# Performance work log

Hardware: AMD Instinct MI355X
Metric: run time of the kernel (lower is better)

The kernel has to match this reference:

```python
import jax, jax.numpy as jnp
import numpy as np

INPUT_DIM = 1024
GRID_SIZE = 5
SPLINE_ORDER = 3
GRID_MIN, GRID_MAX = -1.5, 1.5
NUM_BASIS = GRID_SIZE + SPLINE_ORDER  # 8
LN_EPS = 1e-5


def _spline_grid():
    # grid = arange(-spline_order, grid_size+spline_order+1)*h + grid_min, per input dim
    h = (GRID_MAX - GRID_MIN) / GRID_SIZE
    g = jnp.arange(-SPLINE_ORDER, GRID_SIZE + SPLINE_ORDER + 1, dtype=jnp.float32) * h + GRID_MIN  # [12]
    return jnp.broadcast_to(g, (INPUT_DIM, g.shape[0]))  # [D, 12]


def _rbf_grid():
    return jnp.linspace(GRID_MIN, GRID_MAX, NUM_BASIS, dtype=jnp.float32)  # [8]


def _b_splines(x):
    # x: [B, D] -> bases [B, D, grid_size+spline_order]
    grid = _spline_grid()  # [D, G]
    xe = x[..., None]  # [B, D, 1]
    bases = ((xe >= grid[:, :-1]) & (xe < grid[:, 1:])).astype(x.dtype)  # [B, D, G-1]
    for k in range(1, SPLINE_ORDER + 1):
        left = (xe - grid[:, :-(k + 1)]) / (grid[:, k:-1] - grid[:, :-(k + 1)])
        right = (grid[:, k + 1:] - xe) / (grid[:, k + 1:] - grid[:, 1:-k])
        bases = left * bases[:, :, :-1] + right * bases[:, :, 1:]
    return bases  # [B, D, NUM_BASIS]


def setup_inputs() -> dict:
    key = jax.random.key(0)
    k1, k2, k3 = jax.random.split(key, 3)
    B, D, O = 8192, INPUT_DIM, 1024
    x = jax.random.normal(k1, (B, D), dtype=jnp.float32)
    ln_weight = jnp.ones((D,), dtype=jnp.float32)
    ln_bias = jnp.zeros((D,), dtype=jnp.float32)
    # kaiming_uniform(a=sqrt(5)) ~ U(-1/sqrt(fan_in), 1/sqrt(fan_in))
    base_weight = jax.random.uniform(k2, (O, D), jnp.float32, -1.0, 1.0) / np.sqrt(D)
    spline_weight = jax.random.uniform(k3, (O, D * NUM_BASIS), jnp.float32, -1.0, 1.0) / np.sqrt(D * NUM_BASIS)
    return {"x": x, "ln_weight": ln_weight, "ln_bias": ln_bias,
            "base_weight": base_weight, "spline_weight": spline_weight}


def reference(x, ln_weight, ln_bias, base_weight, spline_weight):
    B = x.shape[0]
    # LayerNorm
    mu = jnp.mean(x, axis=-1, keepdims=True)
    var = jnp.mean((x - mu) ** 2, axis=-1, keepdims=True)
    xn = (x - mu) * jax.lax.rsqrt(var + LN_EPS) * ln_weight + ln_bias  # [B, D]
    # base branch: SiLU + linear
    base_out = jax.nn.silu(xn) @ base_weight.T  # [B, O]
    # spline branch
    spl = _b_splines(xn).reshape(B, -1)  # [B, D*8]
    spline_out = spl @ spline_weight.T
    # rbf branch (same weight)
    denom = (GRID_MAX - GRID_MIN) / (NUM_BASIS - 1)
    rbf = jnp.exp(-(((xn[..., None] - _rbf_grid()) / denom) ** 2)).reshape(B, -1)  # [B, D*8]
    rbf_out = rbf @ spline_weight.T
    return base_out + rbf_out + spline_out
```

## Files before the change

### kernel.cpp

```cpp
#include <hip/hip_runtime.h>

#define B_ROWS 8192
#define D_IN   1024
#define NOUT   1024
#define KB     1024
#define KS     8192
#define GM     256
#define GN     128
#define GK     64
#define GKS    128

#define TBL_N  2048
#define TBL_X0 (-5.5f)
#define TBL_W  11.0f

typedef __attribute__((ext_vector_type(4))) float f32x4;
typedef __attribute__((ext_vector_type(4))) int   i32x4;
typedef __attribute__((ext_vector_type(8))) short bf16x8;

#define SCALE_F 63.5f
#define SCALE_W 11494.728f

__device__ __forceinline__ unsigned short f2bf(float f) {
  union { float f; unsigned u; } v; v.f = f;
  unsigned r = v.u + 0x7fffu + ((v.u >> 16) & 1u);
  return (unsigned short)(r >> 16);
}

__device__ __forceinline__ unsigned pk4(float a, float b, float c, float d, float s) {
  int qa = (int)rintf(fminf(fmaxf(a * s, -127.f), 127.f));
  int qb = (int)rintf(fminf(fmaxf(b * s, -127.f), 127.f));
  int qc = (int)rintf(fminf(fmaxf(c * s, -127.f), 127.f));
  int qd = (int)rintf(fminf(fmaxf(d * s, -127.f), 127.f));
  return (unsigned)(qa & 255) | ((unsigned)(qb & 255) << 8) |
         ((unsigned)(qc & 255) << 16) | ((unsigned)(qd & 255) << 24);
}

__device__ __forceinline__ void load_lds16(const void* g, void* l) {
  __builtin_amdgcn_global_load_lds(
      (const __attribute__((address_space(1))) unsigned int*)g,
      (__attribute__((address_space(3))) unsigned int*)l, 16, 0, 0);
}

__device__ __forceinline__ void barrier_raw() {
  asm volatile("" ::: "memory");
  __builtin_amdgcn_s_barrier();
  asm volatile("" ::: "memory");
}

__global__ __launch_bounds__(256) void tbl_kernel(unsigned char* __restrict__ T) {
  const int k = blockIdx.x * 256 + threadIdx.x;
  const float xn = TBL_X0 + (TBL_W / TBL_N) * k;
  float b[11];
#pragma unroll
  for (int j = 0; j < 11; ++j) {
    const float gj = 0.6f * j - 3.3f;
    b[j] = (xn >= gj && xn < gj + 0.6f) ? 1.f : 0.f;
  }
#pragma unroll
  for (int kk = 1; kk <= 3; ++kk) {
    const float inv = 1.f / (0.6f * kk);
#pragma unroll
    for (int j = 0; j <= 10 - kk; ++j) {
      const float gj = 0.6f * j - 3.3f;
      b[j] = (xn - gj) * inv * b[j] + (gj + 0.6f * (kk + 1) - xn) * inv * b[j + 1];
    }
  }
  float f[8];
#pragma unroll
  for (int j = 0; j < 8; ++j) {
    const float c = -1.5f + (3.f / 7.f) * j;
    const float tt = (xn - c) * (7.f / 3.f);
    f[j] = b[j] + __expf(-tt * tt);
  }
  *reinterpret_cast<uint2*>(T + (size_t)k * 8) =
      make_uint2(pk4(f[0], f[1], f[2], f[3], SCALE_F),
                 pk4(f[4], f[5], f[6], f[7], SCALE_F));
}

__global__ __launch_bounds__(256) void wconv_b(
    const float* __restrict__ bw, unsigned short* __restrict__ Wb) {
  const size_t idx = ((size_t)blockIdx.x * 256 + threadIdx.x) * 4;
  float4 f = *reinterpret_cast<const float4*>(bw + idx);
  union { unsigned short us[4]; uint2 u2; } o;
  o.us[0] = f2bf(f.x); o.us[1] = f2bf(f.y); o.us[2] = f2bf(f.z); o.us[3] = f2bf(f.w);
  *reinterpret_cast<uint2*>(Wb + idx) = o.u2;
}

__global__ __launch_bounds__(256) void wconv_s(
    const float* __restrict__ sw, unsigned char* __restrict__ Ws) {
  const size_t base = ((size_t)blockIdx.x * 256 + threadIdx.x) * 8;
  float4 v0 = *reinterpret_cast<const float4*>(sw + base);
  float4 v1 = *reinterpret_cast<const float4*>(sw + base + 4);
  *reinterpret_cast<uint2*>(Ws + base) =
      make_uint2(pk4(v0.x, v0.y, v0.z, v0.w, SCALE_W),
                 pk4(v1.x, v1.y, v1.z, v1.w, SCALE_W));
}

__global__ __launch_bounds__(256) void feat_kernel(
    const float* __restrict__ x, const float* __restrict__ lnw,
    const float* __restrict__ lnb, const unsigned char* __restrict__ T,
    unsigned short* __restrict__ Fb, unsigned char* __restrict__ Fs, int row0) {
  const int row = row0 + blockIdx.x;
  const float* xr = x + (size_t)row * D_IN;
  const int t = threadIdx.x;
  float v[4];
  float s = 0.f, s2 = 0.f;
#pragma unroll
  for (int i = 0; i < 4; ++i) {
    v[i] = xr[t + 256 * i];
    s += v[i];
    s2 += v[i] * v[i];
  }
#pragma unroll
  for (int off = 32; off > 0; off >>= 1) {
    s += __shfl_xor(s, off);
    s2 += __shfl_xor(s2, off);
  }
  __shared__ float red[8];
  const int wid = t >> 6;
  if ((t & 63) == 0) { red[wid] = s; red[4 + wid] = s2; }
  __syncthreads();
  s  = red[0] + red[1] + red[2] + red[3];
  s2 = red[4] + red[5] + red[6] + red[7];
  const float mu = s * (1.f / D_IN);
  const float var = s2 * (1.f / D_IN) - mu * mu;
  const float rstd = rsqrtf(var + 1e-5f);
  unsigned short* fbr = Fb + (size_t)blockIdx.x * KB;
  unsigned char*  fsr = Fs + (size_t)blockIdx.x * KS;
#pragma unroll
  for (int i = 0; i < 4; ++i) {
    const int d = t + 256 * i;
    const float xn = (v[i] - mu) * rstd * lnw[d] + lnb[d];
    const float e = __expf(-xn);
    fbr[d] = f2bf(xn * __builtin_amdgcn_rcpf(1.f + e));
    int ti = (int)rintf((xn - TBL_X0) * (TBL_N / TBL_W));
    ti = min(max(ti, 0), TBL_N - 1);
    *reinterpret_cast<uint2*>(fsr + d * 8) =
        *reinterpret_cast<const uint2*>(T + (size_t)ti * 8);
  }
}

__global__ __launch_bounds__(512, 2) void gemm_base(
    const unsigned short* __restrict__ A, const unsigned short* __restrict__ Bw,
    float* __restrict__ C, int row0) {
  __shared__ unsigned short As[3][GM * GK];
  __shared__ unsigned short Bs[3][GN * GK];
  const int t = threadIdx.x;
  const int w = t >> 6, l = t & 63;
  const int wr = w >> 1, wc = w & 1;
  const int id = blockIdx.x;
  const int nbm = gridDim.x >> 3;
  int bm, bn;
  if ((nbm & 7) == 0) {
    const int c = id & 7, j = id >> 3, q = nbm >> 3;
    bm = c + 8 * (j % q);
    bn = j / q;
  } else { bm = id % nbm; bn = id / nbm; }
  const size_t Abase = (size_t)bm * GM * KB;
  const size_t Bbase = (size_t)bn * GN * KB;
  const int arow = l >> 3;
  const int achk = (l & 7) ^ arow;
  f32x4 acc[4][4] = {};
  auto stageA = [&](int buf, int k0) {
#pragma unroll
    for (int i = 0; i < 4; ++i) {
      const int seg = w * 4 + i;
      load_lds16(A + Abase + (size_t)(seg * 8 + arow) * KB + k0 + achk * 8,
                 (char*)&As[buf][0] + seg * 1024);
    }
  };
  auto stageB = [&](int buf, int k0) {
#pragma unroll
    for (int i = 0; i < 2; ++i) {
      const int seg = w * 2 + i;
      load_lds16(Bw + Bbase + (size_t)(seg * 8 + arow) * KB + k0 + achk * 8,
                 (char*)&Bs[buf][0] + seg * 1024);
    }
  };
  const int hi = l >> 4;
  const int rA = wr * 64 + (l & 15);
  const int rB = wc * 64 + (l & 15);
  const int rs = l & 7;
  auto dsread = [&](int buf, int kk, bf16x8* a, bf16x8* b) {
    const int cb = ((kk * 4 + hi) ^ rs) * 16;
#pragma unroll
    for (int m = 0; m < 4; ++m)
      a[m] = *reinterpret_cast<const bf16x8*>(
          (const char*)&As[buf][0] + (rA + m * 16) * 128 + cb);
#pragma unroll
    for (int n = 0; n < 4; ++n)
      b[n] = *reinterpret_cast<const bf16x8*>(
          (const char*)&Bs[buf][0] + (rB + n * 16) * 128 + cb);
  };
  auto domfma = [&](bf16x8* a, bf16x8* b) {
    __builtin_amdgcn_s_setprio(1);
#pragma unroll
    for (int m = 0; m < 4; ++m)
#pragma unroll
      for (int n = 0; n < 4; ++n)
        acc[m][n] = __builtin_amdgcn_mfma_f32_16x16x32_bf16(a[m], b[n], acc[m][n], 0, 0, 0);
    __builtin_amdgcn_s_setprio(0);
  };
  const int NT = KB / GK;
  stageA(0, 0); stageB(0, 0);
  stageA(1, GK); stageB(1, GK);
  asm volatile("s_waitcnt vmcnt(6)" ::: "memory");
  barrier_raw();
  int cur = 0;
  for (int tt = 0; tt < NT; ++tt) {
    int pre = cur + 2; if (pre >= 3) pre -= 3;
    const bool have2 = (tt + 2 < NT);
    bf16x8 a0[4], b0[4], a1[4], b1[4];
    dsread(cur, 0, a0, b0);
    dsread(cur, 1, a1, b1);
    if (have2) { stageA(pre, (tt + 2) * GK); stageB(pre, (tt + 2) * GK); }
    __builtin_amdgcn_sched_barrier(0);
    domfma(a0, b0);
    __builtin_amdgcn_sched_barrier(0);
    domfma(a1, b1);
    if (tt + 1 < NT) {
      if (have2) asm volatile("s_waitcnt vmcnt(6)" ::: "memory");
      else       asm volatile("s_waitcnt vmcnt(0)" ::: "memory");
      barrier_raw();
    }
    cur = cur + 1; if (cur >= 3) cur = 0;
  }
  const int crow0 = row0 + bm * GM + wr * 64 + hi * 4;
  const int ccol0 = bn * GN + wc * 64 + (l & 15);
#pragma unroll
  for (int m = 0; m < 4; ++m)
#pragma unroll
    for (int n = 0; n < 4; ++n) {
      float* cp = C + (size_t)(crow0 + m * 16) * NOUT + ccol0 + n * 16;
#pragma unroll
      for (int r = 0; r < 4; ++r)
        cp[(size_t)r * NOUT] = acc[m][n][r];
    }
}

__global__ __launch_bounds__(512, 2) void gemm_spline(
    const unsigned char* __restrict__ Fs, const unsigned char* __restrict__ Ws,
    float* __restrict__ C, int row0) {
  __shared__ __align__(16) unsigned char As[3][GM * GKS];
  __shared__ __align__(16) unsigned char Bs[3][GN * GKS];
  const int t = threadIdx.x;
  const int w = t >> 6, l = t & 63;
  const int wr = w >> 1, wc = w & 1;
  const int id = blockIdx.x;
  const int nbm = gridDim.x >> 3;
  int bm, bn;
  if ((nbm & 7) == 0) {
    const int c = id & 7, j = id >> 3, q = nbm >> 3;
    bm = c + 8 * (j % q);
    bn = j / q;
  } else { bm = id % nbm; bn = id / nbm; }
  const size_t Ab = (size_t)bm * GM * KS;
  const size_t Bb = (size_t)bn * GN * KS;
  i32x4 acc[4][4] = {};
  auto stageA = [&](int buf, int k0) {
#pragma unroll
    for (int i = 0; i < 4; ++i) {
      const int ch = i * 512 + t;
      const int r = ch >> 3, c = ch & 7;
      load_lds16(Fs + Ab + (size_t)r * KS + k0 + ((c ^ (r & 7)) * 16),
                 (char*)&As[buf][0] + ch * 16);
    }
  };
  auto stageB = [&](int buf, int k0) {
#pragma unroll
    for (int i = 0; i < 2; ++i) {
      const int ch = i * 512 + t;
      const int r = ch >> 3, c = ch & 7;
      load_lds16(Ws + Bb + (size_t)r * KS + k0 + ((c ^ (r & 7)) * 16),
                 (char*)&Bs[buf][0] + ch * 16);
    }
  };
  const int hi = l >> 4, l15 = l & 15, rs = l & 7;
  const int c0 = (hi ^ rs) * 16;
  const int c1 = ((4 + hi) ^ rs) * 16;
  i32x4 a0[4], a1[4], b0[4], b1[4];
  auto dsread = [&](int buf) {
    const char* Asb = (const char*)&As[buf][0];
    const char* Bsb = (const char*)&Bs[buf][0];
#pragma unroll
    for (int m = 0; m < 4; ++m) {
      a0[m] = *reinterpret_cast<const i32x4*>(Asb + (wr * 64 + l15 + m * 16) * 128 + c0);
      a1[m] = *reinterpret_cast<const i32x4*>(Asb + (wr * 64 + l15 + m * 16) * 128 + c1);
    }
#pragma unroll
    for (int n = 0; n < 4; ++n) {
      b0[n] = *reinterpret_cast<const i32x4*>(Bsb + (wc * 64 + l15 + n * 16) * 128 + c0);
      b1[n] = *reinterpret_cast<const i32x4*>(Bsb + (wc * 64 + l15 + n * 16) * 128 + c1);
    }
  };
  auto domfma = [&]() {
    __builtin_amdgcn_s_setprio(1);
#pragma unroll
    for (int m = 0; m < 4; ++m)
#pragma unroll
      for (int n = 0; n < 4; ++n)
        acc[m][n] = __builtin_amdgcn_mfma_i32_16x16x64_i8(a0[m], b0[n], acc[m][n], 0, 0, 0);
#pragma unroll
    for (int m = 0; m < 4; ++m)
#pragma unroll
      for (int n = 0; n < 4; ++n)
        acc[m][n] = __builtin_amdgcn_mfma_i32_16x16x64_i8(a1[m], b1[n], acc[m][n], 0, 0, 0);
    __builtin_amdgcn_s_setprio(0);
  };
  const int NT = KS / GKS;
  stageA(0, 0); stageB(0, 0);
  stageA(1, GKS); stageB(1, GKS);
  asm volatile("s_waitcnt vmcnt(6)" ::: "memory");
  barrier_raw();
  int cur = 0;
  for (int tt = 0; tt < NT; ++tt) {
    int pre = cur + 2; if (pre >= 3) pre -= 3;
    const bool have2 = (tt + 2 < NT);
    dsread(cur);
    if (have2) { stageA(pre, (tt + 2) * GKS); stageB(pre, (tt + 2) * GKS); }
    __builtin_amdgcn_sched_barrier(0);
    domfma();
    if (tt + 1 < NT) {
      if (have2) asm volatile("s_waitcnt vmcnt(6)" ::: "memory");
      else       asm volatile("s_waitcnt vmcnt(0)" ::: "memory");
      barrier_raw();
    }
    cur = cur + 1; if (cur >= 3) cur = 0;
  }
  const float sc = 1.0f / (SCALE_F * SCALE_W);
  const int crow0 = row0 + bm * GM + wr * 64 + hi * 4;
  const int ccol0 = bn * GN + wc * 64 + l15;
#pragma unroll
  for (int m = 0; m < 4; ++m)
#pragma unroll
    for (int n = 0; n < 4; ++n) {
      float* cp = C + (size_t)(crow0 + m * 16) * NOUT + ccol0 + n * 16;
#pragma unroll
      for (int r = 0; r < 4; ++r)
        cp[(size_t)r * NOUT] += (float)acc[m][n][r] * sc;
    }
}

extern "C" void kernel_launch(void* const* d_in, const int* in_sizes, int n_in,
                              void* d_out, int out_size, void* d_ws, size_t ws_size,
                              hipStream_t stream) {
  const float* x   = (const float*)d_in[0];
  const float* lnw = (const float*)d_in[1];
  const float* lnb = (const float*)d_in[2];
  const float* bw  = (const float*)d_in[3];
  const float* sw  = (const float*)d_in[4];
  float* out = (float*)d_out;
  char* ws = (char*)d_ws;

  const size_t tbl_bytes = (size_t)TBL_N * 8;
  const size_t wb_bytes = (size_t)NOUT * KB * 2;
  const size_t wsq_bytes = (size_t)NOUT * KS;
  unsigned char*  T   = (unsigned char*)ws;
  unsigned short* Wb  = (unsigned short*)(ws + tbl_bytes);
  unsigned char*  Wsp = (unsigned char*)(ws + tbl_bytes + wb_bytes);
  char* fbase = ws + tbl_bytes + wb_bytes + wsq_bytes;

  const size_t hdr = tbl_bytes + wb_bytes + wsq_bytes;
  const size_t per_row = (size_t)KB * 2 + KS;
  size_t avail = (ws_size > hdr) ? ws_size - hdr : 0;
  long long cm = (long long)(avail / per_row);
  cm &= ~255LL;
  if (cm < 256) cm = 256;
  if (cm > B_ROWS) cm = B_ROWS;
  const int chunkM = (int)cm;
  unsigned short* Fb = (unsigned short*)fbase;
  unsigned char*  Fs = (unsigned char*)(fbase + (size_t)chunkM * KB * 2);

  tbl_kernel<<<TBL_N / 256, 256, 0, stream>>>(T);
  wconv_b<<<(NOUT * KB / 4) / 256, 256, 0, stream>>>(bw, Wb);
  wconv_s<<<(NOUT * KS / 8) / 256, 256, 0, stream>>>(sw, Wsp);
  for (int r0 = 0; r0 < B_ROWS; r0 += chunkM) {
    int rows = B_ROWS - r0; if (rows > chunkM) rows = chunkM;
    feat_kernel<<<rows, 256, 0, stream>>>(x, lnw, lnb, T, Fb, Fs, r0);
    gemm_base<<<dim3((rows / GM) * (NOUT / GN)), 512, 0, stream>>>(Fb, Wb, out, r0);
    gemm_spline<<<dim3((rows / GM) * (NOUT / GN)), 512, 0, stream>>>(Fs, Wsp, out, r0);
  }
}
```

Measured before the change: 122.3 us.

## Fuse base and spline GEMMs into one kernel with a single output write

```diff
diff --git a/kernel.cpp b/kernel.cpp
--- a/kernel.cpp
+++ b/kernel.cpp
@@ -141,11 +141,13 @@
   }
 }
 
-__global__ __launch_bounds__(512, 2) void gemm_base(
-    const unsigned short* __restrict__ A, const unsigned short* __restrict__ Bw,
+__global__ __launch_bounds__(512, 2) void gemm_fused(
+    const unsigned char* __restrict__ Fs, const unsigned char* __restrict__ Ws,
+    const unsigned short* __restrict__ Fb, const unsigned short* __restrict__ Wb,
     float* __restrict__ C, int row0) {
-  __shared__ unsigned short As[3][GM * GK];
-  __shared__ unsigned short Bs[3][GN * GK];
+  __shared__ __align__(16) char smem[3 * 32768 + 3 * 16384];
+  unsigned char* As8 = (unsigned char*)smem;
+  unsigned char* Bs8 = (unsigned char*)(smem + 98304);
   const int t = threadIdx.x;
   const int w = t >> 6, l = t & 63;
   const int wr = w >> 1, wc = w & 1;
@@ -157,177 +159,157 @@
     bm = c + 8 * (j % q);
     bn = j / q;
   } else { bm = id % nbm; bn = id / nbm; }
-  const size_t Abase = (size_t)bm * GM * KB;
-  const size_t Bbase = (size_t)bn * GN * KB;
+
+  const int hi = l >> 4, l15 = l & 15, rs = l & 7;
   const int arow = l >> 3;
   const int achk = (l & 7) ^ arow;
-  f32x4 acc[4][4] = {};
-  auto stageA = [&](int buf, int k0) {
-#pragma unroll
-    for (int i = 0; i < 4; ++i) {
-      const int seg = w * 4 + i;
-      load_lds16(A + Abase + (size_t)(seg * 8 + arow) * KB + k0 + achk * 8,
-                 (char*)&As[buf][0] + seg * 1024);
+
+  i32x4 acc[4][4] = {};
+  {
+    const size_t Ab = (size_t)bm * GM * KS;
+    const size_t Bb = (size_t)bn * GN * KS;
+    auto stageA = [&](int buf, int k0) {
+#pragma unroll
+      for (int i = 0; i < 4; ++i) {
+        const int ch = i * 512 + t;
+        const int r = ch >> 3, c = ch & 7;
+        load_lds16(Fs + Ab + (size_t)r * KS + k0 + ((c ^ (r & 7)) * 16),
+                   As8 + buf * 32768 + ch * 16);
+      }
+    };
+    auto stageB = [&](int buf, int k0) {
+#pragma unroll
+      for (int i = 0; i < 2; ++i) {
+        const int ch = i * 512 + t;
+        const int r = ch >> 3, c = ch & 7;
+        load_lds16(Ws + Bb + (size_t)r * KS + k0 + ((c ^ (r & 7)) * 16),
+                   Bs8 + buf * 16384 + ch * 16);
+      }
+    };
+    const int c0 = (hi ^ rs) * 16;
+    const int c1 = ((4 + hi) ^ rs) * 16;
+    i32x4 a0[4], a1[4], b0[4], b1[4];
+    auto dsread = [&](int buf) {
+      const char* Asb = (const char*)(As8 + buf * 32768);
+      const char* Bsb = (const char*)(Bs8 + buf * 16384);
+#pragma unroll
+      for (int m = 0; m < 4; ++m) {
+        a0[m] = *reinterpret_cast<const i32x4*>(Asb + (wr * 64 + l15 + m * 16) * 128 + c0);
+        a1[m] = *reinterpret_cast<const i32x4*>(Asb + (wr * 64 + l15 + m * 16) * 128 + c1);
+      }
+#pragma unroll
+      for (int n = 0; n < 4; ++n) {
+        b0[n] = *reinterpret_cast<const i32x4*>(Bsb + (wc * 64 + l15 + n * 16) * 128 + c0);
+        b1[n] = *reinterpret_cast<const i32x4*>(Bsb + (wc * 64 + l15 + n * 16) * 128 + c1);
+      }
+    };
+    auto domfma = [&]() {
+      __builtin_amdgcn_s_setprio(1);
+#pragma unroll
+      for (int m = 0; m < 4; ++m)
+#pragma unroll
+        for (int n = 0; n < 4; ++n)
+          acc[m][n] = __builtin_amdgcn_mfma_i32_16x16x64_i8(a0[m], b0[n], acc[m][n], 0, 0, 0);
+#pragma unroll
+      for (int m = 0; m < 4; ++m)
+#pragma unroll
+        for (int n = 0; n < 4; ++n)
+          acc[m][n] = __builtin_amdgcn_mfma_i32_16x16x64_i8(a1[m], b1[n], acc[m][n], 0, 0, 0);
+      __builtin_amdgcn_s_setprio(0);
+    };
+    const int NT = KS / GKS;
+    stageA(0, 0); stageB(0, 0);
+    stageA(1, GKS); stageB(1, GKS);
+    asm volatile("s_waitcnt vmcnt(6)" ::: "memory");
+    barrier_raw();
+    int cur = 0;
+    for (int tt = 0; tt < NT; ++tt) {
+      int pre = cur + 2; if (pre >= 3) pre -= 3;
+      const bool have2 = (tt + 2 < NT);
+      dsread(cur);
+      if (have2) { stageA(pre, (tt + 2) * GKS); stageB(pre, (tt + 2) * GKS); }
+      __builtin_amdgcn_sched_barrier(0);
+      domfma();
+      if (tt + 1 < NT) {
+        if (have2) asm volatile("s_waitcnt vmcnt(6)" ::: "memory");
+        else       asm volatile("s_waitcnt vmcnt(0)" ::: "memory");
+        barrier_raw();
+      }
+      cur = cur + 1; if (cur >= 3) cur = 0;
     }
-  };
-  auto stageB = [&](int buf, int k0) {
-#pragma unroll
-    for (int i = 0; i < 2; ++i) {
-      const int seg = w * 2 + i;
-      load_lds16(Bw + Bbase + (size_t)(seg * 8 + arow) * KB + k0 + achk * 8,
-                 (char*)&Bs[buf][0] + seg * 1024);
+  }
+  barrier_raw();
+
+  f32x4 accf[4][4] = {};
+  {
+    unsigned short* As = (unsigned short*)As8;
+    unsigned short* Bs = (unsigned short*)Bs8;
+    const size_t Abase = (size_t)bm * GM * KB;
+    const size_t Bbase = (size_t)bn * GN * KB;
+    auto stageA = [&](int buf, int k0) {
+#pragma unroll
+      for (int i = 0; i < 4; ++i) {
+        const int seg = w * 4 + i;
+        load_lds16(Fb + Abase + (size_t)(seg * 8 + arow) * KB + k0 + achk * 8,
+                   (char*)(As + buf * 16384) + seg * 1024);
+      }
+    };
+    auto stageB = [&](int buf, int k0) {
+#pragma unroll
+      for (int i = 0; i < 2; ++i) {
+        const int seg = w * 2 + i;
+        load_lds16(Wb + Bbase + (size_t)(seg * 8 + arow) * KB + k0 + achk * 8,
+                   (char*)(Bs + buf * 8192) + seg * 1024);
+      }
+    };
+    const int rA = wr * 64 + l15;
+    const int rB = wc * 64 + l15;
+    auto dsread = [&](int buf, int kk, bf16x8* a, bf16x8* b) {
+      const int cb = ((kk * 4 + hi) ^ rs) * 16;
+#pragma unroll
+      for (int m = 0; m < 4; ++m)
+        a[m] = *reinterpret_cast<const bf16x8*>(
+            (const char*)(As + buf * 16384) + (rA + m * 16) * 128 + cb);
+#pragma unroll
+      for (int n = 0; n < 4; ++n)
+        b[n] = *reinterpret_cast<const bf16x8*>(
+            (const char*)(Bs + buf * 8192) + (rB + n * 16) * 128 + cb);
+    };
+    auto domfma = [&](bf16x8* a, bf16x8* b) {
+      __builtin_amdgcn_s_setprio(1);
+#pragma unroll
+      for (int m = 0; m < 4; ++m)
+#pragma unroll
+        for (int n = 0; n < 4; ++n)
+          accf[m][n] = __builtin_amdgcn_mfma_f32_16x16x32_bf16(a[m], b[n], accf[m][n], 0, 0, 0);
+      __builtin_amdgcn_s_setprio(0);
+    };
+    const int NT = KB / GK;
+    stageA(0, 0); stageB(0, 0);
+    stageA(1, GK); stageB(1, GK);
+    asm volatile("s_waitcnt vmcnt(6)" ::: "memory");
+    barrier_raw();
+    int cur = 0;
+    for (int tt = 0; tt < NT; ++tt) {
+      int pre = cur + 2; if (pre >= 3) pre -= 3;
+      const bool have2 = (tt + 2 < NT);
+      bf16x8 a0[4], b0[4], a1[4], b1[4];
+      dsread(cur, 0, a0, b0);
+      dsread(cur, 1, a1, b1);
+      if (have2) { stageA(pre, (tt + 2) * GK); stageB(pre, (tt + 2) * GK); }
+      __builtin_amdgcn_sched_barrier(0);
+      domfma(a0, b0);
+      __builtin_amdgcn_sched_barrier(0);
+      domfma(a1, b1);
+      if (tt + 1 < NT) {
+        if (have2) asm volatile("s_waitcnt vmcnt(6)" ::: "memory");
+        else       asm volatile("s_waitcnt vmcnt(0)" ::: "memory");
+        barrier_raw();
+      }
+      cur = cur + 1; if (cur >= 3) cur = 0;
     }
-  };
-  const int hi = l >> 4;
-  const int rA = wr * 64 + (l & 15);
-  const int rB = wc * 64 + (l & 15);
-  const int rs = l & 7;
-  auto dsread = [&](int buf, int kk, bf16x8* a, bf16x8* b) {
-    const int cb = ((kk * 4 + hi) ^ rs) * 16;
-#pragma unroll
-    for (int m = 0; m < 4; ++m)
-      a[m] = *reinterpret_cast<const bf16x8*>(
-          (const char*)&As[buf][0] + (rA + m * 16) * 128 + cb);
-#pragma unroll
-    for (int n = 0; n < 4; ++n)
-      b[n] = *reinterpret_cast<const bf16x8*>(
-          (const char*)&Bs[buf][0] + (rB + n * 16) * 128 + cb);
-  };
-  auto domfma = [&](bf16x8* a, bf16x8* b) {
-    __builtin_amdgcn_s_setprio(1);
-#pragma unroll
-    for (int m = 0; m < 4; ++m)
-#pragma unroll
-      for (int n = 0; n < 4; ++n)
-        acc[m][n] = __builtin_amdgcn_mfma_f32_16x16x32_bf16(a[m], b[n], acc[m][n], 0, 0, 0);
-    __builtin_amdgcn_s_setprio(0);
-  };
-  const int NT = KB / GK;
-  stageA(0, 0); stageB(0, 0);
-  stageA(1, GK); stageB(1, GK);
-  asm volatile("s_waitcnt vmcnt(6)" ::: "memory");
-  barrier_raw();
-  int cur = 0;
-  for (int tt = 0; tt < NT; ++tt) {
-    int pre = cur + 2; if (pre >= 3) pre -= 3;
-    const bool have2 = (tt + 2 < NT);
-    bf16x8 a0[4], b0[4], a1[4], b1[4];
-    dsread(cur, 0, a0, b0);
-    dsread(cur, 1, a1, b1);
-    if (have2) { stageA(pre, (tt + 2) * GK); stageB(pre, (tt + 2) * GK); }
-    __builtin_amdgcn_sched_barrier(0);
-    domfma(a0, b0);
-    __builtin_amdgcn_sched_barrier(0);
-    domfma(a1, b1);
-    if (tt + 1 < NT) {
-      if (have2) asm volatile("s_waitcnt vmcnt(6)" ::: "memory");
-      else       asm volatile("s_waitcnt vmcnt(0)" ::: "memory");
-      barrier_raw();
-    }
-    cur = cur + 1; if (cur >= 3) cur = 0;
-  }
-  const int crow0 = row0 + bm * GM + wr * 64 + hi * 4;
-  const int ccol0 = bn * GN + wc * 64 + (l & 15);
-#pragma unroll
-  for (int m = 0; m < 4; ++m)
-#pragma unroll
-    for (int n = 0; n < 4; ++n) {
-      float* cp = C + (size_t)(crow0 + m * 16) * NOUT + ccol0 + n * 16;
-#pragma unroll
-      for (int r = 0; r < 4; ++r)
-        cp[(size_t)r * NOUT] = acc[m][n][r];
-    }
-}
-
-__global__ __launch_bounds__(512, 2) void gemm_spline(
-    const unsigned char* __restrict__ Fs, const unsigned char* __restrict__ Ws,
-    float* __restrict__ C, int row0) {
-  __shared__ __align__(16) unsigned char As[3][GM * GKS];
-  __shared__ __align__(16) unsigned char Bs[3][GN * GKS];
-  const int t = threadIdx.x;
-  const int w = t >> 6, l = t & 63;
-  const int wr = w >> 1, wc = w & 1;
-  const int id = blockIdx.x;
-  const int nbm = gridDim.x >> 3;
-  int bm, bn;
-  if ((nbm & 7) == 0) {
-    const int c = id & 7, j = id >> 3, q = nbm >> 3;
-    bm = c + 8 * (j % q);
-    bn = j / q;
-  } else { bm = id % nbm; bn = id / nbm; }
-  const size_t Ab = (size_t)bm * GM * KS;
-  const size_t Bb = (size_t)bn * GN * KS;
-  i32x4 acc[4][4] = {};
-  auto stageA = [&](int buf, int k0) {
-#pragma unroll
-    for (int i = 0; i < 4; ++i) {
-      const int ch = i * 512 + t;
-      const int r = ch >> 3, c = ch & 7;
-      load_lds16(Fs + Ab + (size_t)r * KS + k0 + ((c ^ (r & 7)) * 16),
-                 (char*)&As[buf][0] + ch * 16);
-    }
-  };
-  auto stageB = [&](int buf, int k0) {
-#pragma unroll
-    for (int i = 0; i < 2; ++i) {
-      const int ch = i * 512 + t;
-      const int r = ch >> 3, c = ch & 7;
-      load_lds16(Ws + Bb + (size_t)r * KS + k0 + ((c ^ (r & 7)) * 16),
-                 (char*)&Bs[buf][0] + ch * 16);
-    }
-  };
-  const int hi = l >> 4, l15 = l & 15, rs = l & 7;
-  const int c0 = (hi ^ rs) * 16;
-  const int c1 = ((4 + hi) ^ rs) * 16;
-  i32x4 a0[4], a1[4], b0[4], b1[4];
-  auto dsread = [&](int buf) {
-    const char* Asb = (const char*)&As[buf][0];
-    const char* Bsb = (const char*)&Bs[buf][0];
-#pragma unroll
-    for (int m = 0; m < 4; ++m) {
-      a0[m] = *reinterpret_cast<const i32x4*>(Asb + (wr * 64 + l15 + m * 16) * 128 + c0);
-      a1[m] = *reinterpret_cast<const i32x4*>(Asb + (wr * 64 + l15 + m * 16) * 128 + c1);
-    }
-#pragma unroll
-    for (int n = 0; n < 4; ++n) {
-      b0[n] = *reinterpret_cast<const i32x4*>(Bsb + (wc * 64 + l15 + n * 16) * 128 + c0);
-      b1[n] = *reinterpret_cast<const i32x4*>(Bsb + (wc * 64 + l15 + n * 16) * 128 + c1);
-    }
-  };
-  auto domfma = [&]() {
-    __builtin_amdgcn_s_setprio(1);
-#pragma unroll
-    for (int m = 0; m < 4; ++m)
-#pragma unroll
-      for (int n = 0; n < 4; ++n)
-        acc[m][n] = __builtin_amdgcn_mfma_i32_16x16x64_i8(a0[m], b0[n], acc[m][n], 0, 0, 0);
-#pragma unroll
-    for (int m = 0; m < 4; ++m)
-#pragma unroll
-      for (int n = 0; n < 4; ++n)
-        acc[m][n] = __builtin_amdgcn_mfma_i32_16x16x64_i8(a1[m], b1[n], acc[m][n], 0, 0, 0);
-    __builtin_amdgcn_s_setprio(0);
-  };
-  const int NT = KS / GKS;
-  stageA(0, 0); stageB(0, 0);
-  stageA(1, GKS); stageB(1, GKS);
-  asm volatile("s_waitcnt vmcnt(6)" ::: "memory");
-  barrier_raw();
-  int cur = 0;
-  for (int tt = 0; tt < NT; ++tt) {
-    int pre = cur + 2; if (pre >= 3) pre -= 3;
-    const bool have2 = (tt + 2 < NT);
-    dsread(cur);
-    if (have2) { stageA(pre, (tt + 2) * GKS); stageB(pre, (tt + 2) * GKS); }
-    __builtin_amdgcn_sched_barrier(0);
-    domfma();
-    if (tt + 1 < NT) {
-      if (have2) asm volatile("s_waitcnt vmcnt(6)" ::: "memory");
-      else       asm volatile("s_waitcnt vmcnt(0)" ::: "memory");
-      barrier_raw();
-    }
-    cur = cur + 1; if (cur >= 3) cur = 0;
-  }
+  }
+
   const float sc = 1.0f / (SCALE_F * SCALE_W);
   const int crow0 = row0 + bm * GM + wr * 64 + hi * 4;
   const int ccol0 = bn * GN + wc * 64 + l15;
@@ -338,7 +320,7 @@
       float* cp = C + (size_t)(crow0 + m * 16) * NOUT + ccol0 + n * 16;
 #pragma unroll
       for (int r = 0; r < 4; ++r)
-        cp[(size_t)r * NOUT] += (float)acc[m][n][r] * sc;
+        cp[(size_t)r * NOUT] = accf[m][n][r] + (float)acc[m][n][r] * sc;
     }
 }
 
@@ -378,7 +360,7 @@
   for (int r0 = 0; r0 < B_ROWS; r0 += chunkM) {
     int rows = B_ROWS - r0; if (rows > chunkM) rows = chunkM;
     feat_kernel<<<rows, 256, 0, stream>>>(x, lnw, lnb, T, Fb, Fs, r0);
-    gemm_base<<<dim3((rows / GM) * (NOUT / GN)), 512, 0, stream>>>(Fb, Wb, out, r0);
-    gemm_spline<<<dim3((rows / GM) * (NOUT / GN)), 512, 0, stream>>>(Fs, Wsp, out, r0);
-  }
-}
+    gemm_fused<<<dim3((rows / GM) * (NOUT / GN)), 512, 0, stream>>>(
+        Fs, Wsp, Fb, Wb, out, r0);
+  }
+}
```

Measured after the change: 112.7 us. 7.8% less time.
